# Kernel tuning notes

Measured on AMD Instinct MI355X. Metric: run time of the kernel, lower is better.

## Reference

```python
import jax, jax.numpy as jnp
import numpy as np

N_SRC = 100_000   # hetero[s].num_nodes
N_DST = 100_000   # hetero[d].num_nodes
E     = 800_000   # edge_index.size(1)
D_SRC = 256       # node_dims['src']
D_DST = 256       # node_dims['dst']
D_REL = 128       # d_rel


def setup_inputs() -> dict:
    key = jax.random.key(0)
    ks = jax.random.split(key, 6)
    x_src = jax.random.normal(ks[0], (N_SRC, D_SRC), jnp.float32)
    x_dst = jax.random.normal(ks[1], (N_DST, D_DST), jnp.float32)
    # nn.Linear(d_in, d_rel, bias=False) weights, stored transposed as [d_in, d_rel]
    W_src = jax.random.normal(ks[2], (D_SRC, D_REL), jnp.float32) / np.sqrt(D_SRC).astype(np.float32)
    W_dst = jax.random.normal(ks[3], (D_DST, D_REL), jnp.float32) / np.sqrt(D_DST).astype(np.float32)
    edge_src = jax.random.randint(ks[4], (E,), 0, N_SRC, jnp.int32)  # edge_index[0]
    edge_dst = jax.random.randint(ks[5], (E,), 0, N_DST, jnp.int32)  # edge_index[1]
    return {"x_src": x_src, "x_dst": x_dst, "W_src": W_src, "W_dst": W_dst,
            "edge_src": edge_src, "edge_dst": edge_dst}


def reference(x_src, x_dst, W_src, W_dst, edge_src, edge_dst):
    # Per-type linear projection (bias-free), as in self.proj[nt](feats)
    p_src = x_src @ W_src            # [N_src, d_rel]
    p_dst = x_dst @ W_dst            # projected per module, unused by this edge type
    del p_dst

    # Degree of each destination (A.sum(dim=1)), clamped to >= 1.
    deg = jax.ops.segment_sum(jnp.ones((E,), jnp.float32), edge_dst,
                              num_segments=N_DST)
    deg = jnp.maximum(deg, 1.0)      # [N_dst]

    # Degree-normalized SpMM: sum of source features per destination / deg.
    # (coalescing duplicate edges sums their unit values; segment_sum matches.)
    agg = jax.ops.segment_sum(p_src[edge_src], edge_dst,
                              num_segments=N_DST)            # [N_dst, d_rel]
    dst = agg / deg[:, None]

    # rel_embs[et] = {'dst': dst, 'src_in': x_proj[s], 'deg_dst': deg}
    return dst, p_src, deg
```

## Files before the change

kernel.cpp:

```cpp
#include <hip/hip_runtime.h>
#include <hip/hip_bf16.h>

#define D_SRC 256
#define D_REL 128

typedef __bf16 bf16x8 __attribute__((ext_vector_type(8)));
typedef float f32x4 __attribute__((ext_vector_type(4)));
typedef float f32x16 __attribute__((ext_vector_type(16)));

__global__ void zero_kernel(int* __restrict__ p, int n) {
    int i = blockIdx.x * 256 + threadIdx.x;
    if (i < n) p[i] = 0;
}

__global__ __launch_bounds__(64) void prep_w_kernel(const float* __restrict__ W,
                                                    bf16x8* __restrict__ Wt) {
    int c = blockIdx.x;
    int ks = c >> 2, n = c & 3;
    int lane = threadIdx.x;
    int col = n * 32 + (lane & 31);
    int k0 = ks * 16 + (lane >> 5) * 8;
    bf16x8 v;
#pragma unroll
    for (int j = 0; j < 8; ++j) v[j] = (__bf16)W[(size_t)(k0 + j) * D_REL + col];
    Wt[c * 64 + lane] = v;
}

__global__ __launch_bounds__(256, 4) void proj_mfma_kernel(
    const float* __restrict__ x, const bf16x8* __restrict__ Wt,
    float* __restrict__ out, unsigned short* __restrict__ out_bf, int M) {
    int tid = threadIdx.x;
    int wave = tid >> 6, lane = tid & 63;
    int half = lane >> 5;
    int r31 = lane & 31;
    int row = blockIdx.x * 128 + wave * 32 + r31;
    int rowc = min(row, M - 1);
    const float* xr = x + (size_t)rowc * D_SRC + half * 8;

    f32x16 acc[4];
#pragma unroll
    for (int n = 0; n < 4; ++n) acc[n] = (f32x16)(0.f);

    f32x4 a0 = *(const f32x4*)(xr);
    f32x4 a1 = *(const f32x4*)(xr + 4);

#pragma unroll
    for (int ks = 0; ks < 16; ++ks) {
        bf16x8 b0 = Wt[(ks * 4 + 0) * 64 + lane];
        bf16x8 b1 = Wt[(ks * 4 + 1) * 64 + lane];
        bf16x8 b2 = Wt[(ks * 4 + 2) * 64 + lane];
        bf16x8 b3 = Wt[(ks * 4 + 3) * 64 + lane];
        f32x4 na0, na1;
        if (ks < 15) {
            na0 = *(const f32x4*)(xr + (ks + 1) * 16);
            na1 = *(const f32x4*)(xr + (ks + 1) * 16 + 4);
        }
        bf16x8 af;
        af[0] = (__bf16)a0[0]; af[1] = (__bf16)a0[1];
        af[2] = (__bf16)a0[2]; af[3] = (__bf16)a0[3];
        af[4] = (__bf16)a1[0]; af[5] = (__bf16)a1[1];
        af[6] = (__bf16)a1[2]; af[7] = (__bf16)a1[3];
        acc[0] = __builtin_amdgcn_mfma_f32_32x32x16_bf16(af, b0, acc[0], 0, 0, 0);
        acc[1] = __builtin_amdgcn_mfma_f32_32x32x16_bf16(af, b1, acc[1], 0, 0, 0);
        acc[2] = __builtin_amdgcn_mfma_f32_32x32x16_bf16(af, b2, acc[2], 0, 0, 0);
        acc[3] = __builtin_amdgcn_mfma_f32_32x32x16_bf16(af, b3, acc[3], 0, 0, 0);
        if (ks < 15) { a0 = na0; a1 = na1; }
    }

    int rbase = blockIdx.x * 128 + wave * 32 + 4 * half;
#pragma unroll
    for (int n = 0; n < 4; ++n) {
#pragma unroll
        for (int reg = 0; reg < 16; ++reg) {
            int r = rbase + (reg & 3) + 8 * (reg >> 2);
            if (r < M) {
                float v = acc[n][reg];
                size_t o = (size_t)r * D_REL + n * 32 + r31;
                out[o] = v;
                out_bf[o] = __bfloat16_as_ushort(__float2bfloat16(v));
            }
        }
    }
}

__global__ void count_kernel(const int* __restrict__ edge_dst, int* __restrict__ deg_i,
                             int* __restrict__ pos_arr, int E) {
    int e = blockIdx.x * 256 + threadIdx.x;
    if (e < E) pos_arr[e] = atomicAdd(&deg_i[edge_dst[e]], 1);
}

__global__ __launch_bounds__(1024) void scan_blocks(
    const int* __restrict__ deg_i, int* __restrict__ incl,
    int* __restrict__ bsums, int n) {
    int i = blockIdx.x * 1024 + threadIdx.x;
    int v = (i < n) ? deg_i[i] : 0;
    int lane = threadIdx.x & 63;
    int wid = threadIdx.x >> 6;
    int x = v;
#pragma unroll
    for (int off = 1; off < 64; off <<= 1) {
        int y = __shfl_up(x, off, 64);
        if (lane >= off) x += y;
    }
    __shared__ int wsum[16];
    if (lane == 63) wsum[wid] = x;
    __syncthreads();
    if (wid == 0 && lane < 16) {
        int s = wsum[lane];
#pragma unroll
        for (int off = 1; off < 16; off <<= 1) {
            int y = __shfl_up(s, off, 64);
            if (lane >= off) s += y;
        }
        wsum[lane] = s;
    }
    __syncthreads();
    int add = (wid > 0) ? wsum[wid - 1] : 0;
    x += add;
    if (i < n) incl[i] = x;
    if (threadIdx.x == 1023) bsums[blockIdx.x] = x;
}

__global__ __launch_bounds__(128) void scan_sums(int* __restrict__ bs, int nb) {
    __shared__ int tmp[128];
    int t = threadIdx.x;
    int v = (t < nb) ? bs[t] : 0;
    tmp[t] = v;
    __syncthreads();
    for (int off = 1; off < 128; off <<= 1) {
        int y = 0;
        if (t >= off) y = tmp[t - off];
        __syncthreads();
        tmp[t] += y;
        __syncthreads();
    }
    if (t < nb) bs[t] = tmp[t] - v;
}

__global__ __launch_bounds__(1024) void finalize_kernel(
    const int* __restrict__ deg_i, const int* __restrict__ incl,
    const int* __restrict__ bsums, int* __restrict__ row_start,
    float* __restrict__ deg_out, int n, int E) {
    int i = blockIdx.x * 1024 + threadIdx.x;
    if (i < n) {
        int off = bsums[blockIdx.x];
        row_start[i] = off + incl[i] - deg_i[i];
        deg_out[i] = (float)max(deg_i[i], 1);
    }
    if (i == 0) row_start[n] = E;
}

__global__ void fill_kernel(const int* __restrict__ edge_src,
                            const int* __restrict__ edge_dst,
                            const int* __restrict__ row_start,
                            const int* __restrict__ pos_arr,
                            int* __restrict__ bucket, int E) {
    int e = blockIdx.x * 256 + threadIdx.x;
    if (e < E) {
        int d = edge_dst[e];
        bucket[row_start[d] + pos_arr[e]] = edge_src[e];
    }
}

__global__ __launch_bounds__(256) void gather_kernel(
    const unsigned int* __restrict__ p_bf, const int* __restrict__ row_start,
    const int* __restrict__ bucket, const float* __restrict__ deg_out,
    float* __restrict__ dst, int n) {
    int row = blockIdx.x * 4 + (threadIdx.x >> 6);
    int lane = threadIdx.x & 63;
    if (row >= n) return;
    int beg = row_start[row], end = row_start[row + 1];
    float ax = 0.f, ay = 0.f;
    int idx = beg;
    for (; idx + 4 <= end; idx += 4) {
        int s0 = bucket[idx + 0];
        int s1 = bucket[idx + 1];
        int s2 = bucket[idx + 2];
        int s3 = bucket[idx + 3];
        unsigned int v0 = p_bf[(size_t)s0 * 64 + lane];
        unsigned int v1 = p_bf[(size_t)s1 * 64 + lane];
        unsigned int v2 = p_bf[(size_t)s2 * 64 + lane];
        unsigned int v3 = p_bf[(size_t)s3 * 64 + lane];
        ax += __uint_as_float(v0 << 16) + __uint_as_float(v1 << 16)
            + __uint_as_float(v2 << 16) + __uint_as_float(v3 << 16);
        ay += __uint_as_float(v0 & 0xffff0000u) + __uint_as_float(v1 & 0xffff0000u)
            + __uint_as_float(v2 & 0xffff0000u) + __uint_as_float(v3 & 0xffff0000u);
    }
    for (; idx < end; ++idx) {
        int s = bucket[idx];
        unsigned int v = p_bf[(size_t)s * 64 + lane];
        ax += __uint_as_float(v << 16);
        ay += __uint_as_float(v & 0xffff0000u);
    }
    float dinv = 1.0f / deg_out[row];
    float2 o;
    o.x = ax * dinv;
    o.y = ay * dinv;
    ((float2*)dst)[(size_t)row * 64 + lane] = o;
}

extern "C" void kernel_launch(void* const* d_in, const int* in_sizes, int n_in,
                              void* d_out, int out_size, void* d_ws, size_t ws_size,
                              hipStream_t stream) {
    const float* x_src = (const float*)d_in[0];
    const float* W_src = (const float*)d_in[2];
    const int* edge_src = (const int*)d_in[4];
    const int* edge_dst = (const int*)d_in[5];

    const int N_SRC = in_sizes[0] / D_SRC;
    const int N_DST = in_sizes[1] / D_SRC;
    const int E = in_sizes[4];

    float* out_dst = (float*)d_out;
    float* out_psrc = out_dst + (size_t)N_DST * D_REL;
    float* out_deg = out_psrc + (size_t)N_SRC * D_REL;

    int* deg_i = (int*)d_ws;
    int* incl = deg_i + N_DST;
    int* row_start = incl + N_DST;
    int* bsums = row_start + N_DST + 1;
    int* pos_arr = bsums + 128;
    int* bucket = pos_arr + E;
    size_t int_bytes = (size_t)(3 * N_DST + 1 + 128 + 2 * (size_t)E) * sizeof(int);
    size_t wt_off = (int_bytes + 255) & ~(size_t)255;
    bf16x8* Wt = (bf16x8*)((char*)d_ws + wt_off);
    size_t pbf_off = wt_off + 65536;
    unsigned short* p_bf = (unsigned short*)((char*)d_ws + pbf_off);

    zero_kernel<<<(N_DST + 255) / 256, 256, 0, stream>>>(deg_i, N_DST);
    prep_w_kernel<<<64, 64, 0, stream>>>(W_src, Wt);
    proj_mfma_kernel<<<(N_SRC + 127) / 128, 256, 0, stream>>>(
        x_src, Wt, out_psrc, p_bf, N_SRC);
    count_kernel<<<(E + 255) / 256, 256, 0, stream>>>(edge_dst, deg_i, pos_arr, E);
    int nb = (N_DST + 1023) / 1024;
    scan_blocks<<<nb, 1024, 0, stream>>>(deg_i, incl, bsums, N_DST);
    scan_sums<<<1, 128, 0, stream>>>(bsums, nb);
    finalize_kernel<<<nb, 1024, 0, stream>>>(deg_i, incl, bsums, row_start, out_deg, N_DST, E);
    fill_kernel<<<(E + 255) / 256, 256, 0, stream>>>(edge_src, edge_dst, row_start, pos_arr, bucket, E);
    gather_kernel<<<(N_DST + 3) / 4, 256, 0, stream>>>(
        (const unsigned int*)p_bf, row_start, bucket, out_deg, out_dst, N_DST);
}
```

Measured before the change: 153.6 us.

## Stage projection input tiles through LDS with async global_load_lds double buffering

```diff
diff --git a/kernel.cpp b/kernel.cpp
--- a/kernel.cpp
+++ b/kernel.cpp
@@ -7,6 +7,9 @@
 typedef __bf16 bf16x8 __attribute__((ext_vector_type(8)));
 typedef float f32x4 __attribute__((ext_vector_type(4)));
 typedef float f32x16 __attribute__((ext_vector_type(16)));
+
+typedef const __attribute__((address_space(1))) void GASV;
+typedef __attribute__((address_space(3))) void LASV;
 
 __global__ void zero_kernel(int* __restrict__ p, int n) {
     int i = blockIdx.x * 256 + threadIdx.x;
@@ -26,48 +29,73 @@
     Wt[c * 64 + lane] = v;
 }
 
-__global__ __launch_bounds__(256, 4) void proj_mfma_kernel(
+__global__ __launch_bounds__(256) void proj_mfma_kernel(
     const float* __restrict__ x, const bf16x8* __restrict__ Wt,
     float* __restrict__ out, unsigned short* __restrict__ out_bf, int M) {
+    __shared__ float lds[2 * 4 * 2048];
     int tid = threadIdx.x;
     int wave = tid >> 6, lane = tid & 63;
-    int half = lane >> 5;
-    int r31 = lane & 31;
-    int row = blockIdx.x * 128 + wave * 32 + r31;
-    int rowc = min(row, M - 1);
-    const float* xr = x + (size_t)rowc * D_SRC + half * 8;
+    int r31 = lane & 31, h = lane >> 5;
+    int row0 = blockIdx.x * 128 + wave * 32;
+
+    float* buf0 = &lds[wave * 2048];
+    float* buf1 = &lds[4 * 2048 + wave * 2048];
+
+    auto stagef = [&](float* dstbase, int kt) {
+#pragma unroll
+        for (int j = 0; j < 8; ++j) {
+            int ci = j * 64 + lane;
+            int rl = ci >> 4;
+            int qql = (ci & 15) ^ ((rl & 7) << 1);
+            int srow = min(row0 + rl, M - 1);
+            const float* src = x + (size_t)srow * D_SRC + kt * 64 + qql * 4;
+            __builtin_amdgcn_global_load_lds((GASV*)src, (LASV*)(dstbase + j * 256),
+                                             16, 0, 0);
+        }
+    };
 
     f32x16 acc[4];
 #pragma unroll
     for (int n = 0; n < 4; ++n) acc[n] = (f32x16)(0.f);
 
-    f32x4 a0 = *(const f32x4*)(xr);
-    f32x4 a1 = *(const f32x4*)(xr + 4);
-
-#pragma unroll
-    for (int ks = 0; ks < 16; ++ks) {
-        bf16x8 b0 = Wt[(ks * 4 + 0) * 64 + lane];
-        bf16x8 b1 = Wt[(ks * 4 + 1) * 64 + lane];
-        bf16x8 b2 = Wt[(ks * 4 + 2) * 64 + lane];
-        bf16x8 b3 = Wt[(ks * 4 + 3) * 64 + lane];
-        f32x4 na0, na1;
-        if (ks < 15) {
-            na0 = *(const f32x4*)(xr + (ks + 1) * 16);
-            na1 = *(const f32x4*)(xr + (ks + 1) * 16 + 4);
-        }
-        bf16x8 af;
-        af[0] = (__bf16)a0[0]; af[1] = (__bf16)a0[1];
-        af[2] = (__bf16)a0[2]; af[3] = (__bf16)a0[3];
-        af[4] = (__bf16)a1[0]; af[5] = (__bf16)a1[1];
-        af[6] = (__bf16)a1[2]; af[7] = (__bf16)a1[3];
-        acc[0] = __builtin_amdgcn_mfma_f32_32x32x16_bf16(af, b0, acc[0], 0, 0, 0);
-        acc[1] = __builtin_amdgcn_mfma_f32_32x32x16_bf16(af, b1, acc[1], 0, 0, 0);
-        acc[2] = __builtin_amdgcn_mfma_f32_32x32x16_bf16(af, b2, acc[2], 0, 0, 0);
-        acc[3] = __builtin_amdgcn_mfma_f32_32x32x16_bf16(af, b3, acc[3], 0, 0, 0);
-        if (ks < 15) { a0 = na0; a1 = na1; }
-    }
-
-    int rbase = blockIdx.x * 128 + wave * 32 + 4 * half;
+    stagef(buf0, 0);
+
+    const float* cur = buf0;
+    float* nxt = buf1;
+#pragma unroll
+    for (int kt = 0; kt < 4; ++kt) {
+        if (kt < 3) {
+            stagef(nxt, kt + 1);
+            asm volatile("s_waitcnt vmcnt(8)" ::: "memory");
+        } else {
+            asm volatile("s_waitcnt vmcnt(0)" ::: "memory");
+        }
+        int sw = (r31 & 7) << 1;
+#pragma unroll
+        for (int st = 0; st < 4; ++st) {
+            int ks = kt * 4 + st;
+            bf16x8 b0 = Wt[(ks * 4 + 0) * 64 + lane];
+            bf16x8 b1 = Wt[(ks * 4 + 1) * 64 + lane];
+            bf16x8 b2 = Wt[(ks * 4 + 2) * 64 + lane];
+            bf16x8 b3 = Wt[(ks * 4 + 3) * 64 + lane];
+            int p0 = (st * 4 + h * 2 + 0) ^ sw;
+            int p1 = (st * 4 + h * 2 + 1) ^ sw;
+            f32x4 a0 = *(const f32x4*)(cur + r31 * 64 + p0 * 4);
+            f32x4 a1 = *(const f32x4*)(cur + r31 * 64 + p1 * 4);
+            bf16x8 af;
+            af[0] = (__bf16)a0[0]; af[1] = (__bf16)a0[1];
+            af[2] = (__bf16)a0[2]; af[3] = (__bf16)a0[3];
+            af[4] = (__bf16)a1[0]; af[5] = (__bf16)a1[1];
+            af[6] = (__bf16)a1[2]; af[7] = (__bf16)a1[3];
+            acc[0] = __builtin_amdgcn_mfma_f32_32x32x16_bf16(af, b0, acc[0], 0, 0, 0);
+            acc[1] = __builtin_amdgcn_mfma_f32_32x32x16_bf16(af, b1, acc[1], 0, 0, 0);
+            acc[2] = __builtin_amdgcn_mfma_f32_32x32x16_bf16(af, b2, acc[2], 0, 0, 0);
+            acc[3] = __builtin_amdgcn_mfma_f32_32x32x16_bf16(af, b3, acc[3], 0, 0, 0);
+        }
+        float* t = (float*)cur; cur = nxt; nxt = t;
+    }
+
+    int rbase = blockIdx.x * 128 + wave * 32 + 4 * h;
 #pragma unroll
     for (int n = 0; n < 4; ++n) {
 #pragma unroll
```

New measurement: 151.1 us. No clear change (-1.6%).
